# Kernel optimization log

Measured on AMD Instinct MI355X. Metric: run time of the kernel, lower is better.

Reference implementation:

```python
import jax, jax.numpy as jnp
import numpy as np

# Paul Kellet pink-noise filter coefficients (verbatim from the torch source)
_A = np.array([0.99886, 0.99332, 0.969, 0.8665, 0.55, -0.7616], dtype=np.float32)   # pole feedback
_C = np.array([0.0555179, 0.0750759, 0.153852, 0.3104856, 0.5329522, -0.016898], dtype=np.float32)  # input gains
_B6_GAIN = 0.115926   # b6 is the previous white sample scaled (one-sample delay)
_DIRECT = 0.5362      # direct white feedthrough
_OUT_GAIN = 0.11


def setup_inputs() -> dict:
    key = jax.random.key(0)
    B, L = 256, 65536
    white = jax.random.normal(key, (B, L), dtype=jnp.float32)
    return {"white": white}


def reference(white):
    """Pink noise via the 6-pole IIR recurrence from SignalGenerator.noise('pink'),
    vectorized over a batch of channels; sequential time handled by lax.scan.
    white: [B, L] -> pink: [B, L]
    """
    B, L = white.shape
    a = jnp.asarray(_A)  # [6]
    c = jnp.asarray(_C)  # [6]

    def step(carry, w_t):
        # carry: (b [B,6] pole states, b6 [B] delayed-white state); w_t: [B]
        b, b6 = carry
        b = a * b + w_t[:, None] * c                      # [B,6]
        pink_t = (b.sum(-1) + b6 + _DIRECT * w_t) * _OUT_GAIN  # [B]
        return (b, _B6_GAIN * w_t), pink_t

    init = (jnp.zeros((B, 6), dtype=white.dtype), jnp.zeros((B,), dtype=white.dtype))
    _, pink_tb = jax.lax.scan(step, init, white.T)  # scan over time: [L, B]
    return pink_tb.T  # [B, L]
```

## Files before the change

kernel.cpp:

```cpp
#include <hip/hip_runtime.h>


constexpr int kL = 65536;
constexpr int kThreads = 512;
constexpr int kChunk = kL / kThreads;
constexpr int kVec = kChunk / 4;

__global__ __launch_bounds__(kThreads) void pink_kernel(
    const float* __restrict__ white, float* __restrict__ pink)
{
    constexpr float A0 = 0.99886f, A1 = 0.99332f, A2 = 0.969f,
                    A3 = 0.8665f,  A4 = 0.55f,    A5 = -0.7616f;
    constexpr float C0 = 0.0555179f, C1 = 0.0750759f, C2 = 0.153852f,
                    C3 = 0.3104856f, C4 = 0.5329522f, C5 = -0.016898f;
    constexpr float B6G = 0.115926f, DIRECT = 0.5362f, OUTG = 0.11f;

    const int ch   = blockIdx.x;
    const int tid  = threadIdx.x;
    const int lane = tid & 63;
    const int wave = tid >> 6;

    const float* __restrict__ wrow = white + (size_t)ch * kL;
    float* __restrict__ prow       = pink  + (size_t)ch * kL;
    const int t0 = tid * kChunk;

    const float4* __restrict__ wv = (const float4*)(wrow + t0);

    float e0 = 0.f, e1 = 0.f, e2 = 0.f, e3 = 0.f, e4 = 0.f, e5 = 0.f;
    {
        auto step1 = [&](float w) {
            e0 = fmaf(A0, e0, w * C0);
            e1 = fmaf(A1, e1, w * C1);
            e2 = fmaf(A2, e2, w * C2);
            e3 = fmaf(A3, e3, w * C3);
            e4 = fmaf(A4, e4, w * C4);
            e5 = fmaf(A5, e5, w * C5);
        };
        #pragma unroll 4
        for (int i = 0; i < kVec; ++i) {
            float4 w4 = wv[i];
            step1(w4.x); step1(w4.y); step1(w4.z); step1(w4.w);
        }
    }

    float m0 = A0, m1 = A1, m2 = A2, m3 = A3, m4 = A4, m5 = A5;
    #pragma unroll
    for (int i = 0; i < 7; ++i) {
        m0 *= m0; m1 *= m1; m2 *= m2; m3 *= m3; m4 *= m4; m5 *= m5;
    }

    #pragma unroll
    for (int off = 1; off < 64; off <<= 1) {
        float fm0 = __shfl_up(m0, off), fe0 = __shfl_up(e0, off);
        float fm1 = __shfl_up(m1, off), fe1 = __shfl_up(e1, off);
        float fm2 = __shfl_up(m2, off), fe2 = __shfl_up(e2, off);
        float fm3 = __shfl_up(m3, off), fe3 = __shfl_up(e3, off);
        float fm4 = __shfl_up(m4, off), fe4 = __shfl_up(e4, off);
        float fm5 = __shfl_up(m5, off), fe5 = __shfl_up(e5, off);
        if (lane >= off) {
            e0 = fmaf(m0, fe0, e0); m0 *= fm0;
            e1 = fmaf(m1, fe1, e1); m1 *= fm1;
            e2 = fmaf(m2, fe2, e2); m2 *= fm2;
            e3 = fmaf(m3, fe3, e3); m3 *= fm3;
            e4 = fmaf(m4, fe4, e4); m4 *= fm4;
            e5 = fmaf(m5, fe5, e5); m5 *= fm5;
        }
    }

    __shared__ float sm[8][6];
    __shared__ float se[8][6];
    if (lane == 63) {
        sm[wave][0] = m0; sm[wave][1] = m1; sm[wave][2] = m2;
        sm[wave][3] = m3; sm[wave][4] = m4; sm[wave][5] = m5;
        se[wave][0] = e0; se[wave][1] = e1; se[wave][2] = e2;
        se[wave][3] = e3; se[wave][4] = e4; se[wave][5] = e5;
    }
    __syncthreads();

    float E0 = 0.f, E1 = 0.f, E2 = 0.f, E3 = 0.f, E4 = 0.f, E5 = 0.f;
    for (int w2 = 0; w2 < wave; ++w2) {
        E0 = fmaf(sm[w2][0], E0, se[w2][0]);
        E1 = fmaf(sm[w2][1], E1, se[w2][1]);
        E2 = fmaf(sm[w2][2], E2, se[w2][2]);
        E3 = fmaf(sm[w2][3], E3, se[w2][3]);
        E4 = fmaf(sm[w2][4], E4, se[w2][4]);
        E5 = fmaf(sm[w2][5], E5, se[w2][5]);
    }

    float xm0 = __shfl_up(m0, 1), xe0 = __shfl_up(e0, 1);
    float xm1 = __shfl_up(m1, 1), xe1 = __shfl_up(e1, 1);
    float xm2 = __shfl_up(m2, 1), xe2 = __shfl_up(e2, 1);
    float xm3 = __shfl_up(m3, 1), xe3 = __shfl_up(e3, 1);
    float xm4 = __shfl_up(m4, 1), xe4 = __shfl_up(e4, 1);
    float xm5 = __shfl_up(m5, 1), xe5 = __shfl_up(e5, 1);
    if (lane == 0) {
        xm0 = 1.f; xe0 = 0.f; xm1 = 1.f; xe1 = 0.f; xm2 = 1.f; xe2 = 0.f;
        xm3 = 1.f; xe3 = 0.f; xm4 = 1.f; xe4 = 0.f; xm5 = 1.f; xe5 = 0.f;
    }

    float b0 = fmaf(xm0, E0, xe0);
    float b1 = fmaf(xm1, E1, xe1);
    float b2 = fmaf(xm2, E2, xe2);
    float b3 = fmaf(xm3, E3, xe3);
    float b4 = fmaf(xm4, E4, xe4);
    float b5 = fmaf(xm5, E5, xe5);

    float b6 = (t0 == 0) ? 0.f : B6G * wrow[t0 - 1];

    float4* __restrict__ pv = (float4*)(prow + t0);
    auto step2 = [&](float w) -> float {
        b0 = fmaf(A0, b0, w * C0);
        b1 = fmaf(A1, b1, w * C1);
        b2 = fmaf(A2, b2, w * C2);
        b3 = fmaf(A3, b3, w * C3);
        b4 = fmaf(A4, b4, w * C4);
        b5 = fmaf(A5, b5, w * C5);
        float s = ((b0 + b1) + (b2 + b3)) + ((b4 + b5) + b6);
        float pk = (s + DIRECT * w) * OUTG;
        b6 = B6G * w;
        return pk;
    };
    #pragma unroll 4
    for (int i = 0; i < kVec; ++i) {
        float4 w4 = wv[i];
        float4 o;
        o.x = step2(w4.x);
        o.y = step2(w4.y);
        o.z = step2(w4.z);
        o.w = step2(w4.w);
        pv[i] = o;
    }
}

extern "C" void kernel_launch(void* const* d_in, const int* in_sizes, int n_in,
                              void* d_out, int out_size, void* d_ws, size_t ws_size,
                              hipStream_t stream) {
    const float* white = (const float*)d_in[0];
    float* pink = (float*)d_out;
    const int B = in_sizes[0] / kL;
    hipLaunchKernelGGL(pink_kernel, dim3(B), dim3(kThreads), 0, stream,
                       white, pink);
}
```

Measured before the change: 133.9 us.

## Split pink-noise scan into two-pass tiled block scan across many blocks

```diff
diff --git a/kernel.cpp b/kernel.cpp
--- a/kernel.cpp
+++ b/kernel.cpp
@@ -2,134 +2,180 @@
 
 
 constexpr int kL = 65536;
-constexpr int kThreads = 512;
-constexpr int kChunk = kL / kThreads;
-constexpr int kVec = kChunk / 4;
+constexpr int kThreads = 1024;
+constexpr int kWaves = kThreads / 64;
+constexpr int kTile = kThreads * 4;
+constexpr int kTilesPerCh = kL / kTile;
 
-__global__ __launch_bounds__(kThreads) void pink_kernel(
-    const float* __restrict__ white, float* __restrict__ pink)
+__device__ __constant__ float dA[6] = {0.99886f, 0.99332f, 0.969f, 0.8665f, 0.55f, -0.7616f};
+__device__ __constant__ float dC[6] = {0.0555179f, 0.0750759f, 0.153852f, 0.3104856f, 0.5329522f, -0.016898f};
+
+__global__ __launch_bounds__(kThreads) void pink_pass1(
+    const float* __restrict__ white, float* __restrict__ blk_e)
 {
-    constexpr float A0 = 0.99886f, A1 = 0.99332f, A2 = 0.969f,
-                    A3 = 0.8665f,  A4 = 0.55f,    A5 = -0.7616f;
-    constexpr float C0 = 0.0555179f, C1 = 0.0750759f, C2 = 0.153852f,
-                    C3 = 0.3104856f, C4 = 0.5329522f, C5 = -0.016898f;
-    constexpr float B6G = 0.115926f, DIRECT = 0.5362f, OUTG = 0.11f;
-
-    const int ch   = blockIdx.x;
     const int tid  = threadIdx.x;
     const int lane = tid & 63;
     const int wave = tid >> 6;
 
-    const float* __restrict__ wrow = white + (size_t)ch * kL;
-    float* __restrict__ prow       = pink  + (size_t)ch * kL;
-    const int t0 = tid * kChunk;
+    const size_t base = (size_t)blockIdx.x * kTile;
+    float4 w4 = ((const float4*)(white + base))[tid];
 
-    const float4* __restrict__ wv = (const float4*)(wrow + t0);
-
-    float e0 = 0.f, e1 = 0.f, e2 = 0.f, e3 = 0.f, e4 = 0.f, e5 = 0.f;
-    {
-        auto step1 = [&](float w) {
-            e0 = fmaf(A0, e0, w * C0);
-            e1 = fmaf(A1, e1, w * C1);
-            e2 = fmaf(A2, e2, w * C2);
-            e3 = fmaf(A3, e3, w * C3);
-            e4 = fmaf(A4, e4, w * C4);
-            e5 = fmaf(A5, e5, w * C5);
-        };
-        #pragma unroll 4
-        for (int i = 0; i < kVec; ++i) {
-            float4 w4 = wv[i];
-            step1(w4.x); step1(w4.y); step1(w4.z); step1(w4.w);
-        }
+    float e[6], m4[6];
+    #pragma unroll
+    for (int p = 0; p < 6; ++p) {
+        const float A = dA[p], C = dC[p];
+        float b = w4.x * C;
+        b = fmaf(A, b, w4.y * C);
+        b = fmaf(A, b, w4.z * C);
+        b = fmaf(A, b, w4.w * C);
+        e[p] = b;
+        float a2 = A * A;
+        m4[p] = a2 * a2;
     }
 
-    float m0 = A0, m1 = A1, m2 = A2, m3 = A3, m4 = A4, m5 = A5;
+    float mk[6];
     #pragma unroll
-    for (int i = 0; i < 7; ++i) {
-        m0 *= m0; m1 *= m1; m2 *= m2; m3 *= m3; m4 *= m4; m5 *= m5;
+    for (int p = 0; p < 6; ++p) mk[p] = m4[p];
+    #pragma unroll
+    for (int k = 0; k < 6; ++k) {
+        const int off = 1 << k;
+        float fe[6];
+        #pragma unroll
+        for (int p = 0; p < 6; ++p) fe[p] = __shfl_up(e[p], off);
+        if (lane >= off) {
+            #pragma unroll
+            for (int p = 0; p < 6; ++p) e[p] = fmaf(mk[p], fe[p], e[p]);
+        }
+        #pragma unroll
+        for (int p = 0; p < 6; ++p) mk[p] *= mk[p];
     }
 
-    #pragma unroll
-    for (int off = 1; off < 64; off <<= 1) {
-        float fm0 = __shfl_up(m0, off), fe0 = __shfl_up(e0, off);
-        float fm1 = __shfl_up(m1, off), fe1 = __shfl_up(e1, off);
-        float fm2 = __shfl_up(m2, off), fe2 = __shfl_up(e2, off);
-        float fm3 = __shfl_up(m3, off), fe3 = __shfl_up(e3, off);
-        float fm4 = __shfl_up(m4, off), fe4 = __shfl_up(e4, off);
-        float fm5 = __shfl_up(m5, off), fe5 = __shfl_up(e5, off);
-        if (lane >= off) {
-            e0 = fmaf(m0, fe0, e0); m0 *= fm0;
-            e1 = fmaf(m1, fe1, e1); m1 *= fm1;
-            e2 = fmaf(m2, fe2, e2); m2 *= fm2;
-            e3 = fmaf(m3, fe3, e3); m3 *= fm3;
-            e4 = fmaf(m4, fe4, e4); m4 *= fm4;
-            e5 = fmaf(m5, fe5, e5); m5 *= fm5;
-        }
-    }
-
-    __shared__ float sm[8][6];
-    __shared__ float se[8][6];
+    __shared__ float se[kWaves][6];
     if (lane == 63) {
-        sm[wave][0] = m0; sm[wave][1] = m1; sm[wave][2] = m2;
-        sm[wave][3] = m3; sm[wave][4] = m4; sm[wave][5] = m5;
-        se[wave][0] = e0; se[wave][1] = e1; se[wave][2] = e2;
-        se[wave][3] = e3; se[wave][4] = e4; se[wave][5] = e5;
+        #pragma unroll
+        for (int p = 0; p < 6; ++p) se[wave][p] = e[p];
     }
     __syncthreads();
 
-    float E0 = 0.f, E1 = 0.f, E2 = 0.f, E3 = 0.f, E4 = 0.f, E5 = 0.f;
-    for (int w2 = 0; w2 < wave; ++w2) {
-        E0 = fmaf(sm[w2][0], E0, se[w2][0]);
-        E1 = fmaf(sm[w2][1], E1, se[w2][1]);
-        E2 = fmaf(sm[w2][2], E2, se[w2][2]);
-        E3 = fmaf(sm[w2][3], E3, se[w2][3]);
-        E4 = fmaf(sm[w2][4], E4, se[w2][4]);
-        E5 = fmaf(sm[w2][5], E5, se[w2][5]);
+    if (tid < 6) {
+        float Mw = m4[tid];
+        #pragma unroll
+        for (int s = 0; s < 6; ++s) Mw *= Mw;
+        float E = 0.f;
+        for (int w = 0; w < kWaves; ++w) E = fmaf(Mw, E, se[w][tid]);
+        blk_e[(size_t)blockIdx.x * 6 + tid] = E;
+    }
+}
+
+__global__ __launch_bounds__(kThreads) void pink_pass2(
+    const float* __restrict__ white, const float* __restrict__ blk_e,
+    float* __restrict__ pink)
+{
+    constexpr float B6G = 0.115926f, DIRECT = 0.5362f, OUTG = 0.11f;
+
+    const int tid  = threadIdx.x;
+    const int lane = tid & 63;
+    const int wave = tid >> 6;
+    const int blk  = blockIdx.x;
+    const int ch   = blk >> 4;
+    const int tile = blk & (kTilesPerCh - 1);
+
+    const size_t base = (size_t)blk * kTile;
+    float4 w4 = ((const float4*)(white + base))[tid];
+
+    float e[6], m4[6];
+    #pragma unroll
+    for (int p = 0; p < 6; ++p) {
+        const float A = dA[p], C = dC[p];
+        float b = w4.x * C;
+        b = fmaf(A, b, w4.y * C);
+        b = fmaf(A, b, w4.z * C);
+        b = fmaf(A, b, w4.w * C);
+        e[p] = b;
+        float a2 = A * A;
+        m4[p] = a2 * a2;
     }
 
-    float xm0 = __shfl_up(m0, 1), xe0 = __shfl_up(e0, 1);
-    float xm1 = __shfl_up(m1, 1), xe1 = __shfl_up(e1, 1);
-    float xm2 = __shfl_up(m2, 1), xe2 = __shfl_up(e2, 1);
-    float xm3 = __shfl_up(m3, 1), xe3 = __shfl_up(e3, 1);
-    float xm4 = __shfl_up(m4, 1), xe4 = __shfl_up(e4, 1);
-    float xm5 = __shfl_up(m5, 1), xe5 = __shfl_up(e5, 1);
-    if (lane == 0) {
-        xm0 = 1.f; xe0 = 0.f; xm1 = 1.f; xe1 = 0.f; xm2 = 1.f; xe2 = 0.f;
-        xm3 = 1.f; xe3 = 0.f; xm4 = 1.f; xe4 = 0.f; xm5 = 1.f; xe5 = 0.f;
+    float mk[6];
+    #pragma unroll
+    for (int p = 0; p < 6; ++p) mk[p] = m4[p];
+    #pragma unroll
+    for (int k = 0; k < 6; ++k) {
+        const int off = 1 << k;
+        float fe[6];
+        #pragma unroll
+        for (int p = 0; p < 6; ++p) fe[p] = __shfl_up(e[p], off);
+        if (lane >= off) {
+            #pragma unroll
+            for (int p = 0; p < 6; ++p) e[p] = fmaf(mk[p], fe[p], e[p]);
+        }
+        #pragma unroll
+        for (int p = 0; p < 6; ++p) mk[p] *= mk[p];
     }
 
-    float b0 = fmaf(xm0, E0, xe0);
-    float b1 = fmaf(xm1, E1, xe1);
-    float b2 = fmaf(xm2, E2, xe2);
-    float b3 = fmaf(xm3, E3, xe3);
-    float b4 = fmaf(xm4, E4, xe4);
-    float b5 = fmaf(xm5, E5, xe5);
+    float ex[6];
+    #pragma unroll
+    for (int p = 0; p < 6; ++p) {
+        ex[p] = __shfl_up(e[p], 1);
+        if (lane == 0) ex[p] = 0.f;
+    }
 
-    float b6 = (t0 == 0) ? 0.f : B6G * wrow[t0 - 1];
+    __shared__ float se[kWaves][6];
+    __shared__ float Tsh[6];
+    if (lane == 63) {
+        #pragma unroll
+        for (int p = 0; p < 6; ++p) se[wave][p] = e[p];
+    }
+    __syncthreads();
 
-    float4* __restrict__ pv = (float4*)(prow + t0);
-    auto step2 = [&](float w) -> float {
-        b0 = fmaf(A0, b0, w * C0);
-        b1 = fmaf(A1, b1, w * C1);
-        b2 = fmaf(A2, b2, w * C2);
-        b3 = fmaf(A3, b3, w * C3);
-        b4 = fmaf(A4, b4, w * C4);
-        b5 = fmaf(A5, b5, w * C5);
-        float s = ((b0 + b1) + (b2 + b3)) + ((b4 + b5) + b6);
+    if (tid < 6) {
+        float Mt = m4[tid];
+        #pragma unroll
+        for (int s = 0; s < 10; ++s) Mt *= Mt;
+        float T = 0.f;
+        const float* ep = blk_e + (size_t)(ch * kTilesPerCh) * 6 + tid;
+        for (int k = 0; k < tile; ++k) T = fmaf(Mt, T, ep[k * 6]);
+        Tsh[tid] = T;
+    }
+    __syncthreads();
+
+    float b[6];
+    #pragma unroll
+    for (int p = 0; p < 6; ++p) {
+        float Mw = m4[p];
+        #pragma unroll
+        for (int s = 0; s < 6; ++s) Mw *= Mw;
+        float Wv = Tsh[p];
+        for (int w2 = 0; w2 < wave; ++w2) Wv = fmaf(Mw, Wv, se[w2][p]);
+        float pm = 1.f, q = m4[p];
+        #pragma unroll
+        for (int bit = 0; bit < 6; ++bit) {
+            if ((lane >> bit) & 1) pm *= q;
+            q *= q;
+        }
+        b[p] = fmaf(pm, Wv, ex[p]);
+    }
+
+    float pw = __shfl_up(w4.w, 1);
+    const size_t g0 = base + (size_t)tid * 4;
+    if (lane == 0) pw = ((g0 & (size_t)(kL - 1)) == 0) ? 0.f : white[g0 - 1];
+    float b6 = B6G * pw;
+
+    auto step = [&](float w) -> float {
+        #pragma unroll
+        for (int p = 0; p < 6; ++p) b[p] = fmaf(dA[p], b[p], w * dC[p]);
+        float s = ((b[0] + b[1]) + (b[2] + b[3])) + ((b[4] + b[5]) + b6);
         float pk = (s + DIRECT * w) * OUTG;
         b6 = B6G * w;
         return pk;
     };
-    #pragma unroll 4
-    for (int i = 0; i < kVec; ++i) {
-        float4 w4 = wv[i];
-        float4 o;
-        o.x = step2(w4.x);
-        o.y = step2(w4.y);
-        o.z = step2(w4.z);
-        o.w = step2(w4.w);
-        pv[i] = o;
-    }
+
+    float4 o;
+    o.x = step(w4.x);
+    o.y = step(w4.y);
+    o.z = step(w4.z);
+    o.w = step(w4.w);
+    ((float4*)(pink + base))[tid] = o;
 }
 
 extern "C" void kernel_launch(void* const* d_in, const int* in_sizes, int n_in,
@@ -137,7 +183,11 @@
                               hipStream_t stream) {
     const float* white = (const float*)d_in[0];
     float* pink = (float*)d_out;
-    const int B = in_sizes[0] / kL;
-    hipLaunchKernelGGL(pink_kernel, dim3(B), dim3(kThreads), 0, stream,
-                       white, pink);
+    float* blk_e = (float*)d_ws;
+    const int nBlocks = in_sizes[0] / kTile;
+
+    hipLaunchKernelGGL(pink_pass1, dim3(nBlocks), dim3(kThreads), 0, stream,
+                       white, blk_e);
+    hipLaunchKernelGGL(pink_pass2, dim3(nBlocks), dim3(kThreads), 0, stream,
+                       white, blk_e, pink);
 }
```

After: 217.2 us. 1.62x slower.
